# Kernel optimization log

Hardware: AMD Instinct MI355X
Metric: run time of the kernel (lower is better)

Reference implementation:

```python
import jax, jax.numpy as jnp
import numpy as np

N_NODES = 100000   # ntoken
D = 128            # ninp
N_EDGES = 1600000  # n_nodes * avg_degree(16)


def setup_inputs() -> dict:
    key = jax.random.key(0)
    k0, k1, k2, k3 = jax.random.split(key, 4)
    # nn.Embedding weight, xavier_normal_ init; row 0 is padding_idx -> zeros
    emb = jax.random.normal(k0, (N_NODES, D), jnp.float32) * np.float32(np.sqrt(2.0 / (N_NODES + D)))
    emb = emb.at[0].set(0.0)
    # GCNConv weights (glorot) and biases (zeros), as in torch_geometric defaults
    W1 = jax.random.normal(k1, (D, 2 * D), jnp.float32) * np.float32(np.sqrt(2.0 / (D + 2 * D)))
    b1 = jnp.zeros((2 * D,), jnp.float32)
    W2 = jax.random.normal(k2, (2 * D, D), jnp.float32) * np.float32(np.sqrt(2.0 / (2 * D + D)))
    b2 = jnp.zeros((D,), jnp.float32)
    edge_index = jax.random.randint(k3, (2, N_EDGES), 0, N_NODES, dtype=jnp.int64)
    return {"emb": emb, "W1": W1, "b1": b1, "W2": W2, "b2": b2, "edge_index": edge_index}


def gcn_conv(x, W, b, src, dst, n):
    """torch_geometric GCNConv: add self-loops, sym deg^{-1/2} norm, edge_weight=1."""
    h = x @ W  # [n, out]
    loop = jnp.arange(n, dtype=src.dtype)
    src2 = jnp.concatenate([src, loop])
    dst2 = jnp.concatenate([dst, loop])
    # degree computed at destination (col) including self-loops
    deg = jax.ops.segment_sum(jnp.ones_like(src2, dtype=h.dtype), dst2, num_segments=n)
    dinv = jnp.where(deg > 0, jax.lax.rsqrt(deg), 0.0)
    norm = dinv[src2] * dinv[dst2]  # [E+n]
    msg = h[src2] * norm[:, None]   # gather + scale (memory-bound)
    out = jax.ops.segment_sum(msg, dst2, num_segments=n)  # scatter-add
    return out + b


def reference(emb, W1, b1, W2, b2, edge_index):
    src, dst = edge_index[0], edge_index[1]
    n = emb.shape[0]
    h = gcn_conv(emb, W1, b1, src, dst, n)   # [N, 2D]; dropout = identity (eval)
    out = gcn_conv(h, W2, b2, src, dst, n)   # [N, D]
    return out
```

## Files before the change

### kernel.cpp

```cpp
#include <hip/hip_runtime.h>

static constexpr int D = 128;
static constexpr int CAP = 64;
static constexpr int NSLICE = 8;
static constexpr int CHUNK = 4096;

typedef __attribute__((ext_vector_type(8))) short bf16x8;
typedef __attribute__((ext_vector_type(4))) float f32x4;
typedef __attribute__((ext_vector_type(4))) int iv4;

__device__ inline unsigned bf16rne(float f) {
  unsigned u = __float_as_uint(f);
  return (u + 0x7FFFu + ((u >> 16) & 1u)) >> 16;
}

__global__ __launch_bounds__(128) void k_w1w2(const float* __restrict__ W1,
                                              const float* __restrict__ W2,
                                              const float* __restrict__ b1,
                                              float* __restrict__ Wc,
                                              float* __restrict__ c2) {
  int r = blockIdx.x, c = threadIdx.x;
  if (r < 128) {
    float acc = 0.f;
    for (int m = 0; m < 256; ++m) acc = fmaf(W1[(size_t)r * 256 + m], W2[(size_t)m * D + c], acc);
    Wc[(size_t)r * D + c] = acc;
  } else {
    float a2 = 0.f;
    for (int m = 0; m < 256; ++m) a2 = fmaf(b1[m], W2[(size_t)m * D + c], a2);
    c2[c] = a2;
  }
}

__global__ __launch_bounds__(256) void k_pack(const float* __restrict__ Wc, uint4* __restrict__ Wp) {
  int t = blockIdx.x * blockDim.x + threadIdx.x;
  if (t >= 2048) return;
  int l = t & 63, g = t >> 6;
  int ct = g >> 2, ks = g & 3;
  int col = ct * 16 + (l & 15);
  int k0 = ks * 32 + (l >> 4) * 8;
  unsigned r[4];
  #pragma unroll
  for (int jj = 0; jj < 4; ++jj) {
    unsigned lo = bf16rne(Wc[(size_t)(k0 + 2 * jj) * D + col]);
    unsigned hi = bf16rne(Wc[(size_t)(k0 + 2 * jj + 1) * D + col]);
    r[jj] = lo | (hi << 16);
  }
  Wp[t] = make_uint4(r[0], r[1], r[2], r[3]);
}

__global__ __launch_bounds__(256) void k_combo(
    const int* __restrict__ src, const int* __restrict__ dst,
    int* __restrict__ cnt, int* __restrict__ ell,
    const float4* __restrict__ emb4, const uint4* __restrict__ Wp,
    ushort* __restrict__ G16, int e, int n, int fillblocks) {
  const int bid = blockIdx.x;
  const int tid = threadIdx.x;

  if (bid < fillblocks) {
    const int slice = bid % NSLICE;
    const int chunk = bid / NSLICE;
    const int lo = (int)((long long)n * slice / NSLICE);
    const int hi = (int)((long long)n * (slice + 1) / NSLICE);
    const int cbase = chunk * CHUNK;
    #pragma unroll
    for (int i = 0; i < 4; ++i) {
      int idx = cbase + i * 1024 + tid * 4;
      if (idx + 4 <= e) {
        iv4 d4 = __builtin_nontemporal_load((const iv4*)(dst + idx));
        iv4 s4 = __builtin_nontemporal_load((const iv4*)(src + idx));
        if (d4.x >= lo && d4.x < hi) { int p = atomicAdd(&cnt[d4.x], 1); if (p < CAP) ell[(size_t)d4.x * CAP + p] = s4.x; }
        if (d4.y >= lo && d4.y < hi) { int p = atomicAdd(&cnt[d4.y], 1); if (p < CAP) ell[(size_t)d4.y * CAP + p] = s4.y; }
        if (d4.z >= lo && d4.z < hi) { int p = atomicAdd(&cnt[d4.z], 1); if (p < CAP) ell[(size_t)d4.z * CAP + p] = s4.z; }
        if (d4.w >= lo && d4.w < hi) { int p = atomicAdd(&cnt[d4.w], 1); if (p < CAP) ell[(size_t)d4.w * CAP + p] = s4.w; }
      } else {
        for (int k = idx; k < e && k < idx + 4; ++k) {
          int s = src[k], d = dst[k];
          if (d >= lo && d < hi) { int p = atomicAdd(&cnt[d], 1); if (p < CAP) ell[(size_t)d * CAP + p] = s; }
        }
      }
    }
  } else {
    const int gb = bid - fillblocks;
    const int wv = tid >> 6;
    const int l = tid & 63;
    const int row0 = gb * 64 + wv * 16;
    const int rA = row0 + (l & 15);
    const int kb = l >> 4;

    bf16x8 afr[4];
    #pragma unroll
    for (int ks = 0; ks < 4; ++ks) {
      bf16x8 a = 0;
      if (rA < n) {
        float4 v0 = emb4[(size_t)rA * 32 + ks * 8 + kb * 2];
        float4 v1 = emb4[(size_t)rA * 32 + ks * 8 + kb * 2 + 1];
        a[0] = (short)bf16rne(v0.x); a[1] = (short)bf16rne(v0.y);
        a[2] = (short)bf16rne(v0.z); a[3] = (short)bf16rne(v0.w);
        a[4] = (short)bf16rne(v1.x); a[5] = (short)bf16rne(v1.y);
        a[6] = (short)bf16rne(v1.z); a[7] = (short)bf16rne(v1.w);
      }
      afr[ks] = a;
    }

    #pragma unroll
    for (int ct = 0; ct < 8; ++ct) {
      f32x4 acc = {0.f, 0.f, 0.f, 0.f};
      #pragma unroll
      for (int ks = 0; ks < 4; ++ks) {
        bf16x8 bfr = *reinterpret_cast<const bf16x8*>(Wp + (size_t)(ct * 4 + ks) * 64 + l);
        acc = __builtin_amdgcn_mfma_f32_16x16x32_bf16(afr[ks], bfr, acc, 0, 0, 0);
      }
      int col = ct * 16 + (l & 15);
      #pragma unroll
      for (int r = 0; r < 4; ++r) {
        int row = row0 + kb * 4 + r;
        if (row < n) G16[(size_t)row * D + col] = (ushort)bf16rne(acc[r]);
      }
    }
  }
}

template<bool OUT32>
__global__ __launch_bounds__(256) void k_agg(const uint2* __restrict__ x,
                                             const int* __restrict__ cnt,
                                             const int* __restrict__ ell,
                                             const float* __restrict__ addv,
                                             uint2* __restrict__ y16,
                                             float4* __restrict__ y32, int n) {
  int t = blockIdx.x * blockDim.x + threadIdx.x;
  int node = t >> 5, lane = t & 31;
  if (node >= n) return;
  int deg = cnt[node];
  float dd = rsqrtf(1.0f + (float)deg);
  int m = deg < CAP ? deg : CAP;
  const int* row = ell + (size_t)node * CAP;

  uint2 qv = x[(size_t)node * 32 + lane];
  float4 acc;
  acc.x = __uint_as_float(qv.x << 16) * dd;
  acc.y = __uint_as_float(qv.x & 0xFFFF0000u) * dd;
  acc.z = __uint_as_float(qv.y << 16) * dd;
  acc.w = __uint_as_float(qv.y & 0xFFFF0000u) * dd;

#define ACC4(Q, W)                                                         \
  acc.x = fmaf(__uint_as_float((Q).x << 16), (W), acc.x);                  \
  acc.y = fmaf(__uint_as_float((Q).x & 0xFFFF0000u), (W), acc.y);          \
  acc.z = fmaf(__uint_as_float((Q).y << 16), (W), acc.z);                  \
  acc.w = fmaf(__uint_as_float((Q).y & 0xFFFF0000u), (W), acc.w)

  int j = 0;
  for (; j + 8 <= m; j += 8) {
    int4 i0 = *(const int4*)(row + j);
    int4 i1 = *(const int4*)(row + j + 4);
    uint2 q0 = x[(size_t)i0.x * 32 + lane];
    uint2 q1 = x[(size_t)i0.y * 32 + lane];
    uint2 q2 = x[(size_t)i0.z * 32 + lane];
    uint2 q3 = x[(size_t)i0.w * 32 + lane];
    uint2 q4 = x[(size_t)i1.x * 32 + lane];
    uint2 q5 = x[(size_t)i1.y * 32 + lane];
    uint2 q6 = x[(size_t)i1.z * 32 + lane];
    uint2 q7 = x[(size_t)i1.w * 32 + lane];
    float w0 = rsqrtf(1.0f + (float)cnt[i0.x]);
    float w1 = rsqrtf(1.0f + (float)cnt[i0.y]);
    float w2 = rsqrtf(1.0f + (float)cnt[i0.z]);
    float w3 = rsqrtf(1.0f + (float)cnt[i0.w]);
    float w4 = rsqrtf(1.0f + (float)cnt[i1.x]);
    float w5 = rsqrtf(1.0f + (float)cnt[i1.y]);
    float w6 = rsqrtf(1.0f + (float)cnt[i1.z]);
    float w7 = rsqrtf(1.0f + (float)cnt[i1.w]);
    ACC4(q0, w0); ACC4(q1, w1); ACC4(q2, w2); ACC4(q3, w3);
    ACC4(q4, w4); ACC4(q5, w5); ACC4(q6, w6); ACC4(q7, w7);
  }
  for (; j < m; ++j) {
    int s0 = row[j];
    uint2 q0 = x[(size_t)s0 * 32 + lane];
    float w0 = rsqrtf(1.0f + (float)cnt[s0]);
    ACC4(q0, w0);
  }
#undef ACC4

  float4 b = ((const float4*)addv)[lane];
  float4 o;
  o.x = fmaf(acc.x, dd, b.x); o.y = fmaf(acc.y, dd, b.y);
  o.z = fmaf(acc.z, dd, b.z); o.w = fmaf(acc.w, dd, b.w);
  if (OUT32) {
    y32[(size_t)node * 32 + lane] = o;
  } else {
    uint2 p;
    p.x = bf16rne(o.x) | (bf16rne(o.y) << 16);
    p.y = bf16rne(o.z) | (bf16rne(o.w) << 16);
    y16[(size_t)node * 32 + lane] = p;
  }
}

extern "C" void kernel_launch(void* const* d_in, const int* in_sizes, int n_in,
                              void* d_out, int out_size, void* d_ws, size_t ws_size,
                              hipStream_t stream) {
  const float* emb = (const float*)d_in[0];
  const float* W1  = (const float*)d_in[1];
  const float* b1  = (const float*)d_in[2];
  const float* W2  = (const float*)d_in[3];
  const float* b2  = (const float*)d_in[4];
  const int*   ei  = (const int*)d_in[5];

  const int n = in_sizes[0] / D;
  const int e = in_sizes[5] / 2;
  const int* src = ei;
  const int* dst = ei + e;

  const int B = 256;
  const int nchunk = (e + CHUNK - 1) / CHUNK;
  const int fillblocks = nchunk * NSLICE;
  const int gemmblocks = (n + 63) / 64;

  char* ws = (char*)d_ws;
  size_t off = 0;
  auto alloc = [&](size_t bytes) { void* p = ws + off; off = (off + bytes + 255) & ~(size_t)255; return p; };
  int*    cnt = (int*)   alloc((size_t)n * 4);
  int*    ell = (int*)   alloc((size_t)n * CAP * 4);
  float*  Wc  = (float*) alloc((size_t)D * D * 4);
  uint4*  Wp  = (uint4*) alloc(2048 * 16);
  float*  c2  = (float*) alloc((size_t)D * 4);
  ushort* G16 = (ushort*)alloc((size_t)n * D * 2);
  ushort* H16 = (ushort*)alloc((size_t)n * D * 2);
  float*  out = (float*)d_out;

  k_w1w2<<<129, 128, 0, stream>>>(W1, W2, b1, Wc, c2);
  k_pack<<<8, B, 0, stream>>>(Wc, Wp);

  (void)hipMemsetAsync(cnt, 0, (size_t)n * 4, stream);
  k_combo<<<fillblocks + gemmblocks, B, 0, stream>>>(src, dst, cnt, ell,
                                                     (const float4*)emb, Wp, G16,
                                                     e, n, fillblocks);

  {
    long long t = (long long)n * 32;
    k_agg<false><<<(int)((t + B - 1) / B), B, 0, stream>>>(
        (const uint2*)G16, cnt, ell, c2, (uint2*)H16, nullptr, n);
  }
  {
    long long t = (long long)n * 32;
    k_agg<true><<<(int)((t + B - 1) / B), B, 0, stream>>>(
        (const uint2*)H16, cnt, ell, b2, nullptr, (float4*)out, n);
  }
}
```

Before: 248.1 us.

## Split feature dimension into panels across blocks in aggregation kernels

The aggregation kernels now split each node's 128 features into 8 column panels, one panel per block, with 4 threads per node and 64 nodes per block. Consecutive blocks cover different panels of the same node group. The aim is to shrink the live gather footprint of each wave to a 32-byte slice per row, so more nodes run concurrently and L2 reuse of the bf16 feature table improves. The cost is that neighbor indices and degree counts are reread 8 times, and each gather touches only a 32-byte sector per neighbor, which weakens coalescing.

```diff
diff --git a/kernel.cpp b/kernel.cpp
--- a/kernel.cpp
+++ b/kernel.cpp
@@ -121,21 +121,26 @@
 }
 
 template<bool OUT32>
-__global__ __launch_bounds__(256) void k_agg(const uint2* __restrict__ x,
-                                             const int* __restrict__ cnt,
-                                             const int* __restrict__ ell,
-                                             const float* __restrict__ addv,
-                                             uint2* __restrict__ y16,
-                                             float4* __restrict__ y32, int n) {
-  int t = blockIdx.x * blockDim.x + threadIdx.x;
-  int node = t >> 5, lane = t & 31;
+__global__ __launch_bounds__(256) void k_aggP(const uint2* __restrict__ x,
+                                              const int* __restrict__ cnt,
+                                              const int* __restrict__ ell,
+                                              const float* __restrict__ addv,
+                                              uint2* __restrict__ y16,
+                                              float4* __restrict__ y32, int n) {
+  const int panel = blockIdx.x % NSLICE;
+  const int grp   = blockIdx.x / NSLICE;
+  const int tid   = threadIdx.x;
+  const int node  = grp * 64 + (tid >> 2);
+  const int c     = tid & 3;
   if (node >= n) return;
+  const int xoff = panel * 4 + c;
+
   int deg = cnt[node];
   float dd = rsqrtf(1.0f + (float)deg);
   int m = deg < CAP ? deg : CAP;
   const int* row = ell + (size_t)node * CAP;
 
-  uint2 qv = x[(size_t)node * 32 + lane];
+  uint2 qv = x[(size_t)node * 32 + xoff];
   float4 acc;
   acc.x = __uint_as_float(qv.x << 16) * dd;
   acc.y = __uint_as_float(qv.x & 0xFFFF0000u) * dd;
@@ -152,14 +157,14 @@
   for (; j + 8 <= m; j += 8) {
     int4 i0 = *(const int4*)(row + j);
     int4 i1 = *(const int4*)(row + j + 4);
-    uint2 q0 = x[(size_t)i0.x * 32 + lane];
-    uint2 q1 = x[(size_t)i0.y * 32 + lane];
-    uint2 q2 = x[(size_t)i0.z * 32 + lane];
-    uint2 q3 = x[(size_t)i0.w * 32 + lane];
-    uint2 q4 = x[(size_t)i1.x * 32 + lane];
-    uint2 q5 = x[(size_t)i1.y * 32 + lane];
-    uint2 q6 = x[(size_t)i1.z * 32 + lane];
-    uint2 q7 = x[(size_t)i1.w * 32 + lane];
+    uint2 q0 = x[(size_t)i0.x * 32 + xoff];
+    uint2 q1 = x[(size_t)i0.y * 32 + xoff];
+    uint2 q2 = x[(size_t)i0.z * 32 + xoff];
+    uint2 q3 = x[(size_t)i0.w * 32 + xoff];
+    uint2 q4 = x[(size_t)i1.x * 32 + xoff];
+    uint2 q5 = x[(size_t)i1.y * 32 + xoff];
+    uint2 q6 = x[(size_t)i1.z * 32 + xoff];
+    uint2 q7 = x[(size_t)i1.w * 32 + xoff];
     float w0 = rsqrtf(1.0f + (float)cnt[i0.x]);
     float w1 = rsqrtf(1.0f + (float)cnt[i0.y]);
     float w2 = rsqrtf(1.0f + (float)cnt[i0.z]);
@@ -173,23 +178,23 @@
   }
   for (; j < m; ++j) {
     int s0 = row[j];
-    uint2 q0 = x[(size_t)s0 * 32 + lane];
+    uint2 q0 = x[(size_t)s0 * 32 + xoff];
     float w0 = rsqrtf(1.0f + (float)cnt[s0]);
     ACC4(q0, w0);
   }
 #undef ACC4
 
-  float4 b = ((const float4*)addv)[lane];
+  float4 b = ((const float4*)addv)[xoff];
   float4 o;
   o.x = fmaf(acc.x, dd, b.x); o.y = fmaf(acc.y, dd, b.y);
   o.z = fmaf(acc.z, dd, b.z); o.w = fmaf(acc.w, dd, b.w);
   if (OUT32) {
-    y32[(size_t)node * 32 + lane] = o;
+    y32[(size_t)node * 32 + xoff] = o;
   } else {
     uint2 p;
     p.x = bf16rne(o.x) | (bf16rne(o.y) << 16);
     p.y = bf16rne(o.z) | (bf16rne(o.w) << 16);
-    y16[(size_t)node * 32 + lane] = p;
+    y16[(size_t)node * 32 + xoff] = p;
   }
 }
 
@@ -212,6 +217,7 @@
   const int nchunk = (e + CHUNK - 1) / CHUNK;
   const int fillblocks = nchunk * NSLICE;
   const int gemmblocks = (n + 63) / 64;
+  const int aggblocks = ((n + 63) / 64) * NSLICE;
 
   char* ws = (char*)d_ws;
   size_t off = 0;
@@ -233,14 +239,9 @@
                                                      (const float4*)emb, Wp, G16,
                                                      e, n, fillblocks);
 
-  {
-    long long t = (long long)n * 32;
-    k_agg<false><<<(int)((t + B - 1) / B), B, 0, stream>>>(
-        (const uint2*)G16, cnt, ell, c2, (uint2*)H16, nullptr, n);
-  }
-  {
-    long long t = (long long)n * 32;
-    k_agg<true><<<(int)((t + B - 1) / B), B, 0, stream>>>(
-        (const uint2*)H16, cnt, ell, b2, nullptr, (float4*)out, n);
-  }
-}
+  k_aggP<false><<<aggblocks, B, 0, stream>>>(
+      (const uint2*)G16, cnt, ell, c2, (uint2*)H16, nullptr, n);
+
+  k_aggP<true><<<aggblocks, B, 0, stream>>>(
+      (const uint2*)H16, cnt, ell, b2, nullptr, (float4*)out, n);
+}
```

After: 562.6 us. 2.27x slower.
